# Performance work log

Measured on AMD Instinct MI355X. Metric: run time of the kernel, lower is better.

The kernel has to match this reference:

```python
import jax, jax.numpy as jnp
import numpy as np
import math

TOP_K = 2
CAPACITY_FACTOR = 1.25


def setup_inputs() -> dict:
    key = jax.random.key(0)
    ks = jax.random.split(key, 5)
    T, H, F, E = 16384, 1024, 4096, 8
    s = lambda d: 1.0 / np.sqrt(d)
    return {
        "tokens": jax.random.normal(ks[0], (T, H), jnp.float32),
        "w_router": jax.random.normal(ks[1], (H, E), jnp.float32) * s(H),
        "w_gate": jax.random.normal(ks[2], (E, H, F), jnp.float32) * s(H),
        "w_up": jax.random.normal(ks[3], (E, H, F), jnp.float32) * s(H),
        "w_down": jax.random.normal(ks[4], (E, F, H), jnp.float32) * s(F),
    }


def _moe_forward(tokens, w_router, w_gate, w_up, w_down):
    T, H = tokens.shape
    E = w_gate.shape[0]
    C = int(math.ceil(CAPACITY_FACTOR * T / E))  # per-expert capacity, static

    # --- Router: softmax over experts, top-k, renormalized weights ---
    logits = tokens @ w_router                       # (T, E)
    probs = jax.nn.softmax(logits, axis=-1)
    topv, topi = jax.lax.top_k(probs, TOP_K)         # (T, K)
    weights = topv / jnp.sum(topv, axis=-1, keepdims=True)

    # --- Dispatch ranks replicating torch loop order: k-slot major, token index minor ---
    onehot = jax.nn.one_hot(topi, E, dtype=jnp.int32)            # (T, K, E)
    counts = onehot.sum(axis=0)                                  # (K, E) tokens per (slot, expert)
    slot_off = jnp.concatenate(
        [jnp.zeros((1, E), jnp.int32), jnp.cumsum(counts, axis=0)[:-1]], axis=0
    )                                                            # (K, E) exclusive offset over k
    rank = jnp.cumsum(onehot, axis=0) - 1 + slot_off[None]       # (T, K, E)
    rank_tk = jnp.take_along_axis(rank, topi[..., None], axis=-1).squeeze(-1)  # (T, K)

    keep = rank_tk < C                                           # tokens beyond capacity are dropped
    slot = jnp.where(keep, rank_tk, C)                           # dropped -> trash slot C

    e_flat = topi.reshape(-1)                                    # (T*K,)
    s_flat = slot.reshape(-1)
    tok_rep = jnp.broadcast_to(tokens[:, None, :], (T, TOP_K, H)).reshape(-1, H)

    # Gather tokens into per-expert capacity buffers (extra trash row at slot C)
    buf = jnp.zeros((E, C + 1, H), tokens.dtype).at[e_flat, s_flat].set(tok_rep)
    x = buf[:, :C]                                               # (E, C, H)

    # --- SwiGLU expert FFN, batched over experts (grouped GEMM) ---
    h = jax.nn.silu(jnp.einsum('ech,ehf->ecf', x, w_gate)) * jnp.einsum('ech,ehf->ecf', x, w_up)
    y = jnp.einsum('ecf,efh->ech', h, w_down)                    # (E, C, H)

    # --- Weighted scatter back to token positions ---
    out_flat = y[e_flat, jnp.minimum(s_flat, C - 1)]             # (T*K, H)
    w_eff = (weights * keep.astype(weights.dtype)).reshape(-1, 1)
    return (out_flat * w_eff).reshape(T, TOP_K, H).sum(axis=1)   # (T, H)


def reference(tokens, w_router, w_gate, w_up, w_down):
    return _moe_forward(tokens, w_router, w_gate, w_up, w_down)
```

## Files before the change

kernel.cpp:

```cpp
#include <hip/hip_runtime.h>
#include <hip/hip_bf16.h>
#include <stdint.h>

#define T_TOK 16384
#define HDIM  1024
#define FDIM  4096
#define NE    8
#define CAP   2560

typedef __attribute__((ext_vector_type(8))) __bf16 bf16x8;
typedef __attribute__((ext_vector_type(4))) float  f32x4;

__device__ __forceinline__ unsigned short f2bf(float f) {
  union { float f; unsigned u; } c; c.f = f;
  unsigned u = c.u;
  return (unsigned short)((u + 0x7FFFu + ((u >> 16) & 1u)) >> 16);
}

__device__ __forceinline__ void gload_lds16(const void* g, void* lds) {
  __builtin_amdgcn_global_load_lds((const __attribute__((address_space(1))) void*)g,
                                   (__attribute__((address_space(3))) void*)lds,
                                   16, 0, 0);
}

__global__ __launch_bounds__(256)
void transpose_cvt(const float* __restrict__ in, unsigned short* __restrict__ out,
                   int R, int Cc) {
  __shared__ unsigned short tile[64][68];
  int e  = blockIdx.z;
  int rb = blockIdx.y << 6, cb = blockIdx.x << 6;
  const float* inp = in + (size_t)e * R * Cc;
  unsigned short* op = out + (size_t)e * R * Cc;
  int lc  = threadIdx.x & 63;
  int lr0 = threadIdx.x >> 6;
#pragma unroll
  for (int rr = 0; rr < 64; rr += 4) {
    int r = rr + lr0;
    float v = inp[(size_t)(rb + r) * Cc + cb + lc];
    tile[lc][r] = f2bf(v);
  }
  __syncthreads();
  int c0 = threadIdx.x >> 3;
  int h0 = (threadIdx.x & 7) << 3;
#pragma unroll
  for (int cc = 0; cc < 64; cc += 32) {
    int c = cc + c0;
    uint2 v0 = *(const uint2*)&tile[c][h0];
    uint2 v1 = *(const uint2*)&tile[c][h0 + 4];
    uint4 v; v.x = v0.x; v.y = v0.y; v.z = v1.x; v.w = v1.y;
    *(uint4*)(op + (size_t)(cb + c) * R + rb + h0) = v;
  }
}

__global__ __launch_bounds__(256)
void transpose_cvt_gu(const float* __restrict__ in, unsigned short* __restrict__ out, int up) {
  __shared__ unsigned short tile[64][68];
  int e  = blockIdx.z;
  int rb = blockIdx.y << 6, cb = blockIdx.x << 6;
  const float* inp = in + (size_t)e * HDIM * FDIM;
  unsigned short* op = out + (size_t)e * 2 * FDIM * HDIM;
  int lc  = threadIdx.x & 63;
  int lr0 = threadIdx.x >> 6;
#pragma unroll
  for (int rr = 0; rr < 64; rr += 4) {
    int r = rr + lr0;
    float v = inp[(size_t)(rb + r) * FDIM + cb + lc];
    tile[lc][r] = f2bf(v);
  }
  __syncthreads();
  int c0 = threadIdx.x >> 3;
  int h0 = (threadIdx.x & 7) << 3;
#pragma unroll
  for (int cc = 0; cc < 64; cc += 32) {
    int c = cc + c0;
    int C = cb + c;
    int orow = ((C >> 5) << 6) + (C & 31) + (up << 5);
    uint2 v0 = *(const uint2*)&tile[c][h0];
    uint2 v1 = *(const uint2*)&tile[c][h0 + 4];
    uint4 v; v.x = v0.x; v.y = v0.y; v.z = v1.x; v.w = v1.y;
    *(uint4*)(op + (size_t)orow * HDIM + rb + h0) = v;
  }
}

__global__ __launch_bounds__(256)
void router_kernel(const float* __restrict__ tokens, const float* __restrict__ wr,
                   int* __restrict__ topsel, float* __restrict__ wts) {
  int lane = threadIdx.x & 63;
  int t = (blockIdx.x << 2) + (threadIdx.x >> 6);
  const float* tok = tokens + (size_t)t * HDIM;
  float acc[8];
#pragma unroll
  for (int i = 0; i < 8; ++i) acc[i] = 0.f;
#pragma unroll
  for (int j = 0; j < 4; ++j) {
    int h0 = j * 256 + lane * 4;
    float4 tv = *(const float4*)(tok + h0);
    const float* w = wr + (size_t)h0 * 8;
#pragma unroll
    for (int q = 0; q < 4; ++q) {
      float xv = ((const float*)&tv)[q];
      float4 wa = *(const float4*)(w + q * 8);
      float4 wb = *(const float4*)(w + q * 8 + 4);
      acc[0] += xv * wa.x; acc[1] += xv * wa.y; acc[2] += xv * wa.z; acc[3] += xv * wa.w;
      acc[4] += xv * wb.x; acc[5] += xv * wb.y; acc[6] += xv * wb.z; acc[7] += xv * wb.w;
    }
  }
#pragma unroll
  for (int off = 1; off < 64; off <<= 1) {
#pragma unroll
    for (int i = 0; i < 8; ++i) acc[i] += __shfl_xor(acc[i], off, 64);
  }
  if (lane == 0) {
    int e0 = 0; float v0 = acc[0];
#pragma unroll
    for (int i = 1; i < 8; ++i) if (acc[i] > v0) { v0 = acc[i]; e0 = i; }
    int e1 = -1; float v1 = -3.4e38f;
#pragma unroll
    for (int i = 0; i < 8; ++i) if (i != e0 && acc[i] > v1) { v1 = acc[i]; e1 = i; }
    float w0 = 1.f / (1.f + __expf(v1 - v0));
    topsel[t * 2] = e0; topsel[t * 2 + 1] = e1;
    wts[t * 2] = w0;    wts[t * 2 + 1] = 1.f - w0;
  }
}

__global__ __launch_bounds__(256)
void dispatch_kernel(const int* __restrict__ topsel, int* __restrict__ slot,
                     int* __restrict__ src_tok) {
  int e = blockIdx.x;
  int w = threadIdx.x >> 6, lane = threadIdx.x & 63;
  __shared__ int gcnt[2][256];
  __shared__ int tot[2];
#pragma unroll
  for (int k = 0; k < 2; ++k)
    for (int g = w; g < 256; g += 4) {
      int ch = topsel[(g * 64 + lane) * 2 + k];
      unsigned long long m = __ballot(ch == e);
      if (lane == 0) gcnt[k][g] = __popcll(m);
    }
  __syncthreads();
  if (w < 2) {
    int k = w;
    int c0 = gcnt[k][lane * 4], c1 = gcnt[k][lane * 4 + 1];
    int c2 = gcnt[k][lane * 4 + 2], c3 = gcnt[k][lane * 4 + 3];
    int s = c0 + c1 + c2 + c3;
    int inc = s;
#pragma unroll
    for (int off = 1; off < 64; off <<= 1) {
      int v = __shfl_up(inc, off, 64);
      if (lane >= off) inc += v;
    }
    int base = inc - s;
    gcnt[k][lane * 4] = base;
    gcnt[k][lane * 4 + 1] = base + c0;
    gcnt[k][lane * 4 + 2] = base + c0 + c1;
    gcnt[k][lane * 4 + 3] = base + c0 + c1 + c2;
    if (lane == 63) tot[k] = inc;
  }
  __syncthreads();
#pragma unroll
  for (int k = 0; k < 2; ++k) {
    int kbase = (k == 1) ? tot[0] : 0;
    for (int g = w; g < 256; g += 4) {
      int t = g * 64 + lane;
      int ch = topsel[t * 2 + k];
      unsigned long long m = __ballot(ch == e);
      if (ch == e) {
        unsigned long long lmask = lane ? (~0ull >> (64 - lane)) : 0ull;
        int r = kbase + gcnt[k][g] + __popcll(m & lmask);
        if (r < CAP) { slot[t * 2 + k] = r; src_tok[e * CAP + r] = t; }
        else         { slot[t * 2 + k] = -1; }
      }
    }
  }
}

__global__ __launch_bounds__(128)
void gather_x(const float* __restrict__ tokens, const int* __restrict__ src_tok,
              unsigned short* __restrict__ x) {
  int s = blockIdx.x;
  int t = src_tok[s];
  unsigned short* xr = x + (size_t)s * HDIM + threadIdx.x * 8;
  uint4 v = {0u, 0u, 0u, 0u};
  if (t >= 0) {
    const float* tr = tokens + (size_t)t * HDIM + threadIdx.x * 8;
    float4 a = *(const float4*)tr;
    float4 b = *(const float4*)(tr + 4);
    v.x = (unsigned)f2bf(a.x) | ((unsigned)f2bf(a.y) << 16);
    v.y = (unsigned)f2bf(a.z) | ((unsigned)f2bf(a.w) << 16);
    v.z = (unsigned)f2bf(b.x) | ((unsigned)f2bf(b.y) << 16);
    v.w = (unsigned)f2bf(b.z) | ((unsigned)f2bf(b.w) << 16);
  }
  *(uint4*)xr = v;
}

template<int MF>
__device__ __forceinline__ void gemm_mainloop(const unsigned short* __restrict__ Ag,
                                              const unsigned short* __restrict__ Bg,
                                              int lda, int ldb, int nkt,
                                              unsigned short* lds, f32x4 (&acc)[MF][4]) {
  constexpr int AEL = MF * 32 * 32;
  constexpr int TEL = AEL + 256 * 32;
  constexpr int NLA = MF / 4;
  constexpr int L   = NLA + 2;
  int tid = threadIdx.x, lane = tid & 63, wid = tid >> 6;
  int wr = wid >> 2, wc = wid & 3, fr = lane & 15, fg = lane >> 4;
  int arow = wr * (MF * 16) + fr;
  int brow = wc * 64 + fr;
  int srow = tid >> 2, sc = (tid & 3) * 8;

  auto stA = [&](int t, int lo) {
    int ks = (t < nkt ? t : nkt - 1) * 32;
    gload_lds16(Ag + (size_t)(lo * 128 + srow) * lda + ks + sc,
                lds + (t % 3) * TEL + (lo * 128 + srow) * 32 + sc);
  };
  auto stB = [&](int t, int lo) {
    int ks = (t < nkt ? t : nkt - 1) * 32;
    gload_lds16(Bg + (size_t)(lo * 128 + srow) * ldb + ks + sc,
                lds + (t % 3) * TEL + AEL + (lo * 128 + srow) * 32 + sc);
  };

#pragma unroll
  for (int t = 0; t < 2; ++t) {
#pragma unroll
    for (int lo = 0; lo < NLA; ++lo) stA(t, lo);
    stB(t, 0); stB(t, 1);
  }
  if constexpr (L == 4) asm volatile("s_waitcnt vmcnt(4)" ::: "memory");
  else                  asm volatile("s_waitcnt vmcnt(3)" ::: "memory");
  __builtin_amdgcn_s_barrier();

  for (int t = 0; t < nkt; ++t) {
    const unsigned short* Ab = lds + (t % 3) * TEL;
    const unsigned short* Bb = Ab + AEL;
    bf16x8 bv[4], af[MF / 2];
#pragma unroll
    for (int n = 0; n < 4; ++n)
      bv[n] = *(const bf16x8*)(Bb + (brow + n * 16) * 32 + fg * 8);
#pragma unroll
    for (int m = 0; m < MF / 2; ++m)
      af[m] = *(const bf16x8*)(Ab + (arow + m * 16) * 32 + fg * 8);
    if constexpr (MF == 8) { stA(t + 2, 0); stA(t + 2, 1); }
    else                   { stA(t + 2, 0); stB(t + 2, 0); }
    __builtin_amdgcn_s_barrier();
    __builtin_amdgcn_s_setprio(1);
#pragma unroll
    for (int m = 0; m < MF / 2; ++m)
#pragma unroll
      for (int n = 0; n < 4; ++n)
        acc[m][n] = __builtin_amdgcn_mfma_f32_16x16x32_bf16(af[m], bv[n], acc[m][n], 0, 0, 0);
    __builtin_amdgcn_s_setprio(0);
    __builtin_amdgcn_s_barrier();
#pragma unroll
    for (int m = 0; m < MF / 2; ++m)
      af[m] = *(const bf16x8*)(Ab + (arow + (MF / 2 + m) * 16) * 32 + fg * 8);
    if constexpr (MF == 8) { stB(t + 2, 0); stB(t + 2, 1); }
    else                   { stB(t + 2, 1); }
    __builtin_amdgcn_s_barrier();
    __builtin_amdgcn_s_setprio(1);
#pragma unroll
    for (int m = 0; m < MF / 2; ++m)
#pragma unroll
      for (int n = 0; n < 4; ++n)
        acc[MF / 2 + m][n] =
            __builtin_amdgcn_mfma_f32_16x16x32_bf16(af[m], bv[n], acc[MF / 2 + m][n], 0, 0, 0);
    __builtin_amdgcn_s_setprio(0);
    if constexpr (L == 4) asm volatile("s_waitcnt vmcnt(4)" ::: "memory");
    else                  asm volatile("s_waitcnt vmcnt(3)" ::: "memory");
    __builtin_amdgcn_s_barrier();
  }
}

__global__ __launch_bounds__(512, 2)
void gemm1_kernel(const unsigned short* __restrict__ x, const unsigned short* __restrict__ wgu,
                  unsigned short* __restrict__ h) {
  __shared__ unsigned short lds[3 * (256 * 32 + 256 * 32)];
  int flat = blockIdx.x;
  int e = flat & 7, idx = flat >> 3;
  int c = idx >> 4, i = idx & 15;
  int cbx = c / 5, cby = c % 5;
  int bx = cbx * 8 + (i & 7), by = cby * 2 + (i >> 3);
  const unsigned short* Ag = x   + ((size_t)e * CAP + (size_t)by * 256) * HDIM;
  const unsigned short* Bg = wgu + ((size_t)e * 2 * FDIM + (size_t)bx * 256) * HDIM;
  f32x4 acc[8][4];
#pragma unroll
  for (int m = 0; m < 8; ++m)
#pragma unroll
    for (int n = 0; n < 4; ++n) acc[m][n] = (f32x4){0.f, 0.f, 0.f, 0.f};
  gemm_mainloop<8>(Ag, Bg, HDIM, HDIM, HDIM / 32, lds, acc);

  int lane = threadIdx.x & 63, wid = threadIdx.x >> 6;
  int wr = wid >> 2, wc = wid & 3, fr = lane & 15, fg = lane >> 4;
  size_t rbase = (size_t)e * CAP + by * 256 + wr * 128 + fg * 4;
  int cb = bx * 128 + wc * 32 + fr;
#pragma unroll
  for (int m = 0; m < 8; ++m)
#pragma unroll
    for (int n = 0; n < 2; ++n)
#pragma unroll
      for (int v = 0; v < 4; ++v) {
        float g = acc[m][n][v], u = acc[m][n + 2][v];
        float s = g / (1.f + __expf(-g));
        h[(rbase + m * 16 + v) * FDIM + cb + n * 16] = f2bf(s * u);
      }
}

__global__ __launch_bounds__(512, 4)
void gemm2_kernel(const unsigned short* __restrict__ h, const unsigned short* __restrict__ wdT,
                  float* __restrict__ y) {
  __shared__ unsigned short lds[3 * (128 * 32 + 256 * 32)];
  int flat = blockIdx.x;
  int e = flat & 7, idx = flat >> 3;
  int bx = idx & 3, by = idx >> 2;
  const unsigned short* Ag = h   + ((size_t)e * CAP  + (size_t)by * 128) * FDIM;
  const unsigned short* Bg = wdT + ((size_t)e * HDIM + (size_t)bx * 256) * FDIM;
  f32x4 acc[4][4];
#pragma unroll
  for (int m = 0; m < 4; ++m)
#pragma unroll
    for (int n = 0; n < 4; ++n) acc[m][n] = (f32x4){0.f, 0.f, 0.f, 0.f};
  gemm_mainloop<4>(Ag, Bg, FDIM, FDIM, FDIM / 32, lds, acc);

  int lane = threadIdx.x & 63, wid = threadIdx.x >> 6;
  int wr = wid >> 2, wc = wid & 3, fr = lane & 15, fg = lane >> 4;
  size_t rbase = (size_t)e * CAP + by * 128 + wr * 64 + fg * 4;
  int cb = bx * 256 + wc * 64 + fr;
#pragma unroll
  for (int m = 0; m < 4; ++m)
#pragma unroll
    for (int n = 0; n < 4; ++n)
#pragma unroll
      for (int v = 0; v < 4; ++v)
        y[(rbase + m * 16 + v) * HDIM + cb + n * 16] = acc[m][n][v];
}

__global__ __launch_bounds__(256)
void combine_kernel(const float* __restrict__ y, const int* __restrict__ topsel,
                    const int* __restrict__ slot, const float* __restrict__ wts,
                    float* __restrict__ out) {
  int t = blockIdx.x;
  int i = threadIdx.x * 4;
  float4 s = {0.f, 0.f, 0.f, 0.f};
#pragma unroll
  for (int k = 0; k < 2; ++k) {
    int sl = slot[t * 2 + k];
    if (sl >= 0) {
      int e = topsel[t * 2 + k];
      float w = wts[t * 2 + k];
      float4 v = *(const float4*)(y + ((size_t)e * CAP + sl) * HDIM + i);
      s.x += w * v.x; s.y += w * v.y; s.z += w * v.z; s.w += w * v.w;
    }
  }
  *(float4*)(out + (size_t)t * HDIM + i) = s;
}

extern "C" void kernel_launch(void* const* d_in, const int* in_sizes, int n_in,
                              void* d_out, int out_size, void* d_ws, size_t ws_size,
                              hipStream_t stream) {
  const float* tokens   = (const float*)d_in[0];
  const float* w_router = (const float*)d_in[1];
  const float* w_gate   = (const float*)d_in[2];
  const float* w_up     = (const float*)d_in[3];
  const float* w_down   = (const float*)d_in[4];
  float* out = (float*)d_out;
  char* ws = (char*)d_ws;

  const size_t WGU = (size_t)NE * 2 * FDIM * HDIM * 2;
  const size_t WD  = (size_t)NE * HDIM * FDIM * 2;
  const size_t XB  = (size_t)NE * CAP * HDIM * 2;
  const size_t HB  = (size_t)NE * CAP * FDIM * 2;
  unsigned short* wguT = (unsigned short*)(ws);
  unsigned short* wdT  = (unsigned short*)(ws + WGU);
  unsigned short* xbuf = (unsigned short*)(ws + WGU + WD);
  unsigned short* hbuf = (unsigned short*)(ws + WGU + WD + XB);
  float* ybuf = (float*)(ws);
  char* tail = ws + WGU + WD + XB + HB;
  int*   topsel  = (int*)tail;
  float* wtsv    = (float*)(tail + (size_t)T_TOK * 2 * 4);
  int*   slotv   = (int*)(tail + (size_t)T_TOK * 2 * 8);
  int*   src_tok = (int*)(tail + (size_t)T_TOK * 2 * 12);

  hipMemsetAsync(src_tok, 0xFF, (size_t)NE * CAP * 4, stream);

  transpose_cvt_gu<<<dim3(FDIM / 64, HDIM / 64, NE), 256, 0, stream>>>(w_gate, wguT, 0);
  transpose_cvt_gu<<<dim3(FDIM / 64, HDIM / 64, NE), 256, 0, stream>>>(w_up,   wguT, 1);
  transpose_cvt<<<dim3(HDIM / 64, FDIM / 64, NE), 256, 0, stream>>>(w_down, wdT, FDIM, HDIM);

  router_kernel<<<T_TOK / 4, 256, 0, stream>>>(tokens, w_router, topsel, wtsv);
  dispatch_kernel<<<NE, 256, 0, stream>>>(topsel, slotv, src_tok);
  gather_x<<<NE * CAP, 128, 0, stream>>>(tokens, src_tok, xbuf);

  gemm1_kernel<<<2560, 512, 0, stream>>>(xbuf, wguT, hbuf);
  gemm2_kernel<<<640, 512, 0, stream>>>(hbuf, wdT, ybuf);

  combine_kernel<<<T_TOK, 256, 0, stream>>>(ybuf, topsel, slotv, wtsv, out);
}
```

Baseline: 839.2 us.

## Restructure expert GEMMs into 8-wave quadrant schedule with swizzled BK=64 LDS tiles

Replaces the shared GEMM mainloop with a new 8-wave pipeline that uses a K-tile of 64, double buffering and an XOR-swizzled LDS layout to avoid bank conflicts. Each iteration computes four quadrant sub-products and interleaves fragment loads, async global-to-LDS loads and MFMA issue, with explicit vmcnt waits between them. gemm2 changes to 256x128 tiles with a grouped block ordering, and both kernels drop to one block per CU. The aim is more MFMA work per barrier and fewer LDS conflicts, at the cost of lower occupancy and tighter dependence on the hand-tuned vmcnt counts being correct.

```diff
diff --git a/kernel.cpp b/kernel.cpp
--- a/kernel.cpp
+++ b/kernel.cpp
@@ -10,6 +10,10 @@
 
 typedef __attribute__((ext_vector_type(8))) __bf16 bf16x8;
 typedef __attribute__((ext_vector_type(4))) float  f32x4;
+
+#define MFMA_BF16 __builtin_amdgcn_mfma_f32_16x16x32_bf16
+#define VMCNT(n)  asm volatile("s_waitcnt vmcnt(" #n ")" ::: "memory")
+#define BAR()     __builtin_amdgcn_s_barrier()
 
 __device__ __forceinline__ unsigned short f2bf(float f) {
   union { float f; unsigned u; } c; c.f = f;
@@ -193,87 +197,108 @@
   *(uint4*)xr = v;
 }
 
-template<int MF>
-__device__ __forceinline__ void gemm_mainloop(const unsigned short* __restrict__ Ag,
-                                              const unsigned short* __restrict__ Bg,
-                                              int lda, int ldb, int nkt,
-                                              unsigned short* lds, f32x4 (&acc)[MF][4]) {
-  constexpr int AEL = MF * 32 * 32;
-  constexpr int TEL = AEL + 256 * 32;
-  constexpr int NLA = MF / 4;
-  constexpr int L   = NLA + 2;
+template<int BN>
+__device__ __forceinline__ void mainloop8(const unsigned short* __restrict__ Ag,
+                                          const unsigned short* __restrict__ Bg,
+                                          int lda, int ldb, int nkt,
+                                          unsigned short* lds, f32x4 (&acc)[4][BN / 32]) {
+  constexpr int NF  = BN / 64;
+  constexpr int AEL = 256 * 64;
+  constexpr int BEL = BN * 64;
   int tid = threadIdx.x, lane = tid & 63, wid = tid >> 6;
-  int wr = wid >> 2, wc = wid & 3, fr = lane & 15, fg = lane >> 4;
-  int arow = wr * (MF * 16) + fr;
-  int brow = wc * 64 + fr;
-  int srow = tid >> 2, sc = (tid & 3) * 8;
-
-  auto stA = [&](int t, int lo) {
-    int ks = (t < nkt ? t : nkt - 1) * 32;
-    gload_lds16(Ag + (size_t)(lo * 128 + srow) * lda + ks + sc,
-                lds + (t % 3) * TEL + (lo * 128 + srow) * 32 + sc);
-  };
-  auto stB = [&](int t, int lo) {
-    int ks = (t < nkt ? t : nkt - 1) * 32;
-    gload_lds16(Bg + (size_t)(lo * 128 + srow) * ldb + ks + sc,
-                lds + (t % 3) * TEL + AEL + (lo * 128 + srow) * 32 + sc);
-  };
-
-#pragma unroll
-  for (int t = 0; t < 2; ++t) {
-#pragma unroll
-    for (int lo = 0; lo < NLA; ++lo) stA(t, lo);
-    stB(t, 0); stB(t, 1);
-  }
-  if constexpr (L == 4) asm volatile("s_waitcnt vmcnt(4)" ::: "memory");
-  else                  asm volatile("s_waitcnt vmcnt(3)" ::: "memory");
-  __builtin_amdgcn_s_barrier();
+  int qr = wid >> 1, qc = wid & 1;
+  int fr = lane & 15, fg = lane >> 4;
+
+  auto stA = [&](int t, int mh) {
+    int kt = (t < nkt ? t : nkt - 1) * 64;
+    unsigned short* dst = lds + (t & 1) * AEL + mh * 8192;
+#pragma unroll
+    for (int l = 0; l < 2; ++l) {
+      int idx = l * 512 + tid;
+      int row = idx >> 3;
+      int sl  = (idx & 7) ^ (row & 7);
+      gload_lds16(Ag + (size_t)(mh * 128 + row) * lda + kt + sl * 8, dst + idx * 8);
+    }
+  };
+  auto stB = [&](int t, int nh) {
+    int kt = (t < nkt ? t : nkt - 1) * 64;
+    unsigned short* dst = lds + 2 * AEL + (t & 1) * BEL + nh * (BN / 2) * 64;
+#pragma unroll
+    for (int l = 0; l < BN / 128; ++l) {
+      int idx = l * 512 + tid;
+      int row = idx >> 3;
+      int sl  = (idx & 7) ^ (row & 7);
+      gload_lds16(Bg + (size_t)(nh * (BN / 2) + row) * ldb + kt + sl * 8, dst + idx * 8);
+    }
+  };
+
+  const unsigned short* Ab = lds;
+  const unsigned short* Bb = lds + 2 * AEL;
+  auto ldfrag = [&](const unsigned short* buf, int row, int kk) -> bf16x8 {
+    return *(const bf16x8*)(buf + row * 64 + ((((kk << 2) | fg) ^ (row & 7)) << 3));
+  };
+  bf16x8 afr[2][2], bfr[NF][2];
+  auto loadA = [&](int mh) {
+#pragma unroll
+    for (int mf = 0; mf < 2; ++mf)
+#pragma unroll
+      for (int kk = 0; kk < 2; ++kk)
+        afr[mf][kk] = ldfrag(Ab, mh * 128 + qr * 32 + mf * 16 + fr, kk);
+  };
+  auto loadB = [&](int nh) {
+#pragma unroll
+    for (int nf = 0; nf < NF; ++nf)
+#pragma unroll
+      for (int kk = 0; kk < 2; ++kk)
+        bfr[nf][kk] = ldfrag(Bb, nh * (BN / 2) + qc * (NF * 16) + nf * 16 + fr, kk);
+  };
+  auto mmac = [&](int mh, int nh) {
+    __builtin_amdgcn_s_setprio(1);
+#pragma unroll
+    for (int mf = 0; mf < 2; ++mf)
+#pragma unroll
+      for (int nf = 0; nf < NF; ++nf)
+#pragma unroll
+        for (int kk = 0; kk < 2; ++kk)
+          acc[mh * 2 + mf][nh * NF + nf] =
+              MFMA_BF16(afr[mf][kk], bfr[nf][kk], acc[mh * 2 + mf][nh * NF + nf], 0, 0, 0);
+    __builtin_amdgcn_s_setprio(0);
+  };
+
+  stA(0, 0); stB(0, 0); stB(0, 1); stA(0, 1); stA(1, 0); stB(1, 1);
+  if constexpr (BN == 256) VMCNT(8); else VMCNT(6);
+  BAR();
 
   for (int t = 0; t < nkt; ++t) {
-    const unsigned short* Ab = lds + (t % 3) * TEL;
-    const unsigned short* Bb = Ab + AEL;
-    bf16x8 bv[4], af[MF / 2];
-#pragma unroll
-    for (int n = 0; n < 4; ++n)
-      bv[n] = *(const bf16x8*)(Bb + (brow + n * 16) * 32 + fg * 8);
-#pragma unroll
-    for (int m = 0; m < MF / 2; ++m)
-      af[m] = *(const bf16x8*)(Ab + (arow + m * 16) * 32 + fg * 8);
-    if constexpr (MF == 8) { stA(t + 2, 0); stA(t + 2, 1); }
-    else                   { stA(t + 2, 0); stB(t + 2, 0); }
-    __builtin_amdgcn_s_barrier();
-    __builtin_amdgcn_s_setprio(1);
-#pragma unroll
-    for (int m = 0; m < MF / 2; ++m)
-#pragma unroll
-      for (int n = 0; n < 4; ++n)
-        acc[m][n] = __builtin_amdgcn_mfma_f32_16x16x32_bf16(af[m], bv[n], acc[m][n], 0, 0, 0);
-    __builtin_amdgcn_s_setprio(0);
-    __builtin_amdgcn_s_barrier();
-#pragma unroll
-    for (int m = 0; m < MF / 2; ++m)
-      af[m] = *(const bf16x8*)(Ab + (arow + (MF / 2 + m) * 16) * 32 + fg * 8);
-    if constexpr (MF == 8) { stB(t + 2, 0); stB(t + 2, 1); }
-    else                   { stB(t + 2, 1); }
-    __builtin_amdgcn_s_barrier();
-    __builtin_amdgcn_s_setprio(1);
-#pragma unroll
-    for (int m = 0; m < MF / 2; ++m)
-#pragma unroll
-      for (int n = 0; n < 4; ++n)
-        acc[MF / 2 + m][n] =
-            __builtin_amdgcn_mfma_f32_16x16x32_bf16(af[m], bv[n], acc[MF / 2 + m][n], 0, 0, 0);
-    __builtin_amdgcn_s_setprio(0);
-    if constexpr (L == 4) asm volatile("s_waitcnt vmcnt(4)" ::: "memory");
-    else                  asm volatile("s_waitcnt vmcnt(3)" ::: "memory");
-    __builtin_amdgcn_s_barrier();
-  }
-}
-
-__global__ __launch_bounds__(512, 2)
+    Ab = lds + (t & 1) * AEL;
+    Bb = lds + 2 * AEL + (t & 1) * BEL;
+    loadA(0); loadB(0); stB(t + 1, 0);
+    BAR();
+    mmac(0, 0);
+    if constexpr (BN == 256) VMCNT(6); else VMCNT(4);
+    BAR();
+    loadB(1); stA(t + 1, 1);
+    BAR();
+    mmac(0, 1);
+    if constexpr (BN == 256) VMCNT(6); else VMCNT(4);
+    BAR();
+    loadA(1); stA(t + 2, 0);
+    BAR();
+    mmac(1, 1);
+    if constexpr (BN == 256) VMCNT(6); else VMCNT(5);
+    BAR();
+    loadB(0); stB(t + 2, 1);
+    BAR();
+    mmac(1, 0);
+    if constexpr (BN == 256) VMCNT(6); else VMCNT(5);
+    BAR();
+  }
+}
+
+__global__ __launch_bounds__(512, 1)
 void gemm1_kernel(const unsigned short* __restrict__ x, const unsigned short* __restrict__ wgu,
                   unsigned short* __restrict__ h) {
-  __shared__ unsigned short lds[3 * (256 * 32 + 256 * 32)];
+  __shared__ unsigned short lds[2 * 256 * 64 + 2 * 256 * 64];
   int flat = blockIdx.x;
   int e = flat & 7, idx = flat >> 3;
   int c = idx >> 4, i = idx & 15;
@@ -281,56 +306,66 @@
   int bx = cbx * 8 + (i & 7), by = cby * 2 + (i >> 3);
   const unsigned short* Ag = x   + ((size_t)e * CAP + (size_t)by * 256) * HDIM;
   const unsigned short* Bg = wgu + ((size_t)e * 2 * FDIM + (size_t)bx * 256) * HDIM;
-  f32x4 acc[8][4];
-#pragma unroll
-  for (int m = 0; m < 8; ++m)
-#pragma unroll
-    for (int n = 0; n < 4; ++n) acc[m][n] = (f32x4){0.f, 0.f, 0.f, 0.f};
-  gemm_mainloop<8>(Ag, Bg, HDIM, HDIM, HDIM / 32, lds, acc);
+  f32x4 acc[4][8];
+#pragma unroll
+  for (int m = 0; m < 4; ++m)
+#pragma unroll
+    for (int n = 0; n < 8; ++n) acc[m][n] = (f32x4){0.f, 0.f, 0.f, 0.f};
+  mainloop8<256>(Ag, Bg, HDIM, HDIM, HDIM / 64, lds, acc);
 
   int lane = threadIdx.x & 63, wid = threadIdx.x >> 6;
-  int wr = wid >> 2, wc = wid & 3, fr = lane & 15, fg = lane >> 4;
-  size_t rbase = (size_t)e * CAP + by * 256 + wr * 128 + fg * 4;
-  int cb = bx * 128 + wc * 32 + fr;
-#pragma unroll
-  for (int m = 0; m < 8; ++m)
-#pragma unroll
-    for (int n = 0; n < 2; ++n)
-#pragma unroll
-      for (int v = 0; v < 4; ++v) {
-        float g = acc[m][n][v], u = acc[m][n + 2][v];
-        float s = g / (1.f + __expf(-g));
-        h[(rbase + m * 16 + v) * FDIM + cb + n * 16] = f2bf(s * u);
+  int qr = wid >> 1, qc = wid & 1, fr = lane & 15, fg = lane >> 4;
+  size_t rbase = (size_t)e * CAP + by * 256;
+#pragma unroll
+  for (int mi = 0; mi < 4; ++mi) {
+    int row0 = (mi >> 1) * 128 + qr * 32 + (mi & 1) * 16 + fg * 4;
+#pragma unroll
+    for (int nh = 0; nh < 2; ++nh)
+#pragma unroll
+      for (int nf = 0; nf < 2; ++nf) {
+        int fcol = bx * 128 + (nh * 2 + qc) * 32 + nf * 16 + fr;
+#pragma unroll
+        for (int v = 0; v < 4; ++v) {
+          float g = acc[mi][nh * 4 + nf][v];
+          float u = acc[mi][nh * 4 + nf + 2][v];
+          float s = g / (1.f + __expf(-g));
+          h[(rbase + row0 + v) * FDIM + fcol] = f2bf(s * u);
+        }
       }
-}
-
-__global__ __launch_bounds__(512, 4)
+  }
+}
+
+__global__ __launch_bounds__(512, 1)
 void gemm2_kernel(const unsigned short* __restrict__ h, const unsigned short* __restrict__ wdT,
                   float* __restrict__ y) {
-  __shared__ unsigned short lds[3 * (128 * 32 + 256 * 32)];
+  __shared__ unsigned short lds[2 * 256 * 64 + 2 * 128 * 64];
   int flat = blockIdx.x;
   int e = flat & 7, idx = flat >> 3;
-  int bx = idx & 3, by = idx >> 2;
-  const unsigned short* Ag = h   + ((size_t)e * CAP  + (size_t)by * 128) * FDIM;
-  const unsigned short* Bg = wdT + ((size_t)e * HDIM + (size_t)bx * 256) * FDIM;
+  int c = idx >> 4, i = idx & 15;
+  int bx = i & 7, by = c * 2 + (i >> 3);
+  const unsigned short* Ag = h   + ((size_t)e * CAP  + (size_t)by * 256) * FDIM;
+  const unsigned short* Bg = wdT + ((size_t)e * HDIM + (size_t)bx * 128) * FDIM;
   f32x4 acc[4][4];
 #pragma unroll
   for (int m = 0; m < 4; ++m)
 #pragma unroll
     for (int n = 0; n < 4; ++n) acc[m][n] = (f32x4){0.f, 0.f, 0.f, 0.f};
-  gemm_mainloop<4>(Ag, Bg, FDIM, FDIM, FDIM / 32, lds, acc);
+  mainloop8<128>(Ag, Bg, FDIM, FDIM, FDIM / 64, lds, acc);
 
   int lane = threadIdx.x & 63, wid = threadIdx.x >> 6;
-  int wr = wid >> 2, wc = wid & 3, fr = lane & 15, fg = lane >> 4;
-  size_t rbase = (size_t)e * CAP + by * 128 + wr * 64 + fg * 4;
-  int cb = bx * 256 + wc * 64 + fr;
-#pragma unroll
-  for (int m = 0; m < 4; ++m)
-#pragma unroll
-    for (int n = 0; n < 4; ++n)
+  int qr = wid >> 1, qc = wid & 1, fr = lane & 15, fg = lane >> 4;
+  size_t rbase = (size_t)e * CAP + by * 256;
+#pragma unroll
+  for (int mi = 0; mi < 4; ++mi) {
+    int row0 = (mi >> 1) * 128 + qr * 32 + (mi & 1) * 16 + fg * 4;
+#pragma unroll
+    for (int ni = 0; ni < 4; ++ni) {
+      int col = bx * 128 + (ni >> 1) * 64 + qc * 32 + (ni & 1) * 16 + fr;
 #pragma unroll
       for (int v = 0; v < 4; ++v)
-        y[(rbase + m * 16 + v) * HDIM + cb + n * 16] = acc[m][n][v];
+        y[(rbase + row0 + v) * HDIM + col] = acc[mi][ni][v];
+    }
+  }
 }
 
 __global__ __launch_bounds__(256)
```

Measured after the change: 805.6 us. 4.0% less time.
